# Kernel tuning notes

Measured on AMD Instinct MI355X. Metric: run time of the kernel, lower is better.

The kernel has to match this reference:

```python
import jax, jax.numpy as jnp
import numpy as np

E = 512    # len_embeddings
T = 32     # tokennum
H = 256    # hidden_unit
IT = 5     # ICI iterations
B = 4096   # batch
EPS = 1e-6


def setup_inputs() -> dict:
    key = jax.random.key(0)
    k0, k1, k2, k3, k4 = jax.random.split(key, 5)
    x = jax.random.normal(k0, (B, E), dtype=jnp.float32)
    glorot = np.sqrt(2.0 / (E + H)).astype(np.float32)
    w_in = jax.random.normal(k1, (T, E, H), dtype=jnp.float32) * glorot
    w_val = jax.random.normal(k2, (T, E, H), dtype=jnp.float32) * glorot
    # alphas: per-token, per-iteration inhibition strengths (trained; sample nonzero)
    alphas = jax.random.uniform(k3, (T, IT), dtype=jnp.float32) * 0.5
    # scales: per-token output scale (init 1.0, perturb slightly)
    scales = 1.0 + 0.1 * jax.random.normal(k4, (T, H), dtype=jnp.float32)
    gamma = jnp.ones((T, H), dtype=jnp.float32)
    beta = jnp.zeros((T, H), dtype=jnp.float32)
    return {"x": x, "w_in": w_in, "w_val": w_val, "alphas": alphas,
            "scales": scales, "gamma": gamma, "beta": beta}


def reference(x, w_in, w_val, alphas, scales, gamma, beta):
    # batched per-token projection: [B,E] x [T,E,H] -> [B,T,H]
    hidden = jnp.einsum('be,teh->bth', x, w_in)
    # iterative competitive inhibition (fixed small IT loop)
    x_t = jax.nn.relu(hidden)
    for i in range(alphas.shape[1]):
        m = jnp.mean(x_t, axis=-1, keepdims=True)          # [B,T,1]
        a = alphas[:, i][None, :, None]                     # [1,T,1]
        x_t = jax.nn.relu(x_t - a * m)
    sparse_g = scales[None] * x_t                           # [B,T,H]
    # gated value path
    value = jnp.einsum('be,teh->bth', x, w_val)
    s = sparse_g * value
    # per-token LayerNorm over hidden dim, eps=1e-6
    mu = jnp.mean(s, axis=-1, keepdims=True)
    var = jnp.mean((s - mu) ** 2, axis=-1, keepdims=True)
    out = (s - mu) / jnp.sqrt(var + EPS) * gamma[None] + beta[None]
    return out  # [B, T, H]
```

## Files before the change

### kernel.cpp

```cpp
#include <hip/hip_runtime.h>
#include <cstdint>

using u16 = unsigned short;
using u32 = unsigned int;

constexpr int kB  = 4096;
constexpr int kE  = 512;
constexpr int kT  = 32;
constexpr int kH  = 256;
constexpr int kIT = 5;
constexpr float kEPS = 1e-6f;

typedef __attribute__((ext_vector_type(8)))  short short8;
typedef __attribute__((ext_vector_type(16))) float floatx16;
typedef __attribute__((ext_vector_type(8)))  u16   ushort8;
typedef __attribute__((ext_vector_type(4)))  float floatv4;

__device__ __forceinline__ u16 f2bf(float f) {
  u32 u = __builtin_bit_cast(u32, f);
  return (u16)((u + 0x7fffu + ((u >> 16) & 1u)) >> 16);
}

__device__ __forceinline__ floatx16 mfma32(short8 a, short8 b, floatx16 c) {
  return __builtin_amdgcn_mfma_f32_32x32x16_bf16(a, b, c, 0, 0, 0);
}

__device__ __forceinline__ void ntstore4(float* p, float4 v) {
  __builtin_nontemporal_store(__builtin_bit_cast(floatv4, v), (floatv4*)p);
}

__global__ __launch_bounds__(256) void pack_x_kernel(
    const float* __restrict__ x, u16* __restrict__ xp) {
  __shared__ __attribute__((aligned(16))) float tile[64 * 132];
  const int slab = blockIdx.x >> 2;
  const int kg   = blockIdx.x & 3;
  const int tid  = threadIdx.x;

  const int r0 = tid >> 5;
  const int c0 = (tid & 31) * 4;
#pragma unroll
  for (int p = 0; p < 8; ++p) {
    const int r = p * 8 + r0;
    const float4 v = *(const float4*)(x + (size_t)(slab * 64 + r) * kE + kg * 128 + c0);
    *(float4*)(tile + r * 132 + c0) = v;
  }
  __syncthreads();

  const int wv = tid >> 6, lane = tid & 63;
#pragma unroll
  for (int q = 0; q < 4; ++q) {
    const int cc   = wv * 4 + q;
    const int ks_l = cc >> 1;
    const int mt   = cc & 1;
    const int rl   = mt * 32 + (lane & 31);
    const int kl   = ks_l * 16 + (lane >> 5) * 8;
    const float4 f0 = *(const float4*)(tile + rl * 132 + kl);
    const float4 f1 = *(const float4*)(tile + rl * 132 + kl + 4);
    ushort8 o;
    o[0] = f2bf(f0.x); o[1] = f2bf(f0.y); o[2] = f2bf(f0.z); o[3] = f2bf(f0.w);
    o[4] = f2bf(f1.x); o[5] = f2bf(f1.y); o[6] = f2bf(f1.z); o[7] = f2bf(f1.w);
    const int c = slab * 64 + (kg * 8 + ks_l) * 2 + mt;
    *(ushort8*)(xp + (size_t)c * 512 + lane * 8) = o;
  }
}

__global__ __launch_bounds__(256) void pack_w_kernel(
    const float* __restrict__ w_in, const float* __restrict__ w_val,
    u16* __restrict__ wp) {
  __shared__ __attribute__((aligned(16))) float tile[64 * 68];
  const int wb   = blockIdx.x;
  const int tl   = wb & 31;
  const int et   = tl >> 2;
  const int ht   = tl & 3;
  const int tm   = wb >> 5;
  const int t    = tm >> 1, mat = tm & 1;
  const int tid  = threadIdx.x;
  const float* src = (mat ? w_val : w_in) + (size_t)t * kE * kH +
                     (size_t)(et * 64) * kH + ht * 64;
  const int lrow = tid >> 4, lc4 = (tid & 15) * 4;
#pragma unroll
  for (int p = 0; p < 4; ++p) {
    const int e = lrow + p * 16;
    const float4 v = *(const float4*)(src + (size_t)e * kH + lc4);
    tile[e * 68 + lc4 + 0] = v.x; tile[e * 68 + lc4 + 1] = v.y;
    tile[e * 68 + lc4 + 2] = v.z; tile[e * 68 + lc4 + 3] = v.w;
  }
  __syncthreads();
  const int ks_l = tid >> 6, lane = tid & 63;
  const int kloc = ks_l * 16 + (lane >> 5) * 8;
#pragma unroll
  for (int nt_l = 0; nt_l < 2; ++nt_l) {
    const int nloc = nt_l * 32 + (lane & 31);
    ushort8 o;
#pragma unroll
    for (int j = 0; j < 8; ++j) o[j] = f2bf(tile[(kloc + j) * 68 + nloc]);
    const int c = t * 512 + (et * 4 + ks_l) * 16 + (ht * 2 + nt_l) * 2 + mat;
    *(ushort8*)(wp + (size_t)c * 512 + lane * 8) = o;
  }
}

__global__ __launch_bounds__(512, 4) void fused_kernel(
    const u16* __restrict__ xp, const u16* __restrict__ wp,
    const float* __restrict__ alphas, const float* __restrict__ scales,
    const float* __restrict__ gamma, const float* __restrict__ beta,
    float* __restrict__ out) {
  __shared__ __attribute__((aligned(16))) float sAcc[32 * 256];

  const int tid  = threadIdx.x;
  const int wv   = tid >> 6;
  const int lane = tid & 63;
  const int l31  = lane & 31;
  const int h    = lane >> 5;

  const int bid  = blockIdx.x;
  const int xcd  = bid & 7;
  const int r_   = bid >> 3;
  const int st   = r_ >> 6;
  const int wi   = r_ & 63;
  const int t    = xcd * 4 + (wi >> 4);
  const int slab = st * 16 + (wi & 15);

  const u16* xsrc = xp + (size_t)slab * (32 * 2 * 512) + lane * 8;
  const u16* bsrc = wp + (size_t)t * (32 * 16 * 512) + (size_t)(wv * 2) * 512 + lane * 8;

  floatx16 ai[2], av[2];
#pragma unroll
  for (int m = 0; m < 2; ++m) { ai[m] = (floatx16)0.f; av[m] = (floatx16)0.f; }

  short8 A0[2], A1[2], BI[2], BV[2];
#pragma unroll
  for (int pb = 0; pb < 2; ++pb) {
    A0[pb] = *(const short8*)(xsrc + pb * 1024);
    A1[pb] = *(const short8*)(xsrc + pb * 1024 + 512);
    BI[pb] = *(const short8*)(bsrc + (size_t)pb * 8192);
    BV[pb] = *(const short8*)(bsrc + (size_t)pb * 8192 + 512);
  }

#pragma unroll
  for (int p = 0; p < 32; ++p) {
    const int cur = p & 1;
    ai[0] = mfma32(A0[cur], BI[cur], ai[0]);
    ai[1] = mfma32(A1[cur], BI[cur], ai[1]);
    av[0] = mfma32(A0[cur], BV[cur], av[0]);
    av[1] = mfma32(A1[cur], BV[cur], av[1]);
    if (p < 30) {
      A0[cur] = *(const short8*)(xsrc + (p + 2) * 1024);
      A1[cur] = *(const short8*)(xsrc + (p + 2) * 1024 + 512);
      BI[cur] = *(const short8*)(bsrc + (size_t)(p + 2) * 8192);
      BV[cur] = *(const short8*)(bsrc + (size_t)(p + 2) * 8192 + 512);
    }
  }

  const float inv_h = 1.0f / kH;
  float al[kIT];
#pragma unroll
  for (int i = 0; i < kIT; ++i) al[i] = alphas[t * kIT + i] * inv_h;

  const int row_r = tid >> 4;
  const int seg   = tid & 15;
  const int r4    = (row_r & 7) << 2;

#pragma unroll
  for (int mt = 0; mt < 2; ++mt) {
    __syncthreads();
#pragma unroll
    for (int q = 0; q < 16; ++q) {
      const int r   = (q & 3) + 8 * (q >> 2) + 4 * h;
      const int col = wv * 32 + l31;
      sAcc[r * 256 + (col ^ ((r & 7) << 2))] = ai[mt][q];
    }
    __syncthreads();

    float4 xt[4];
#pragma unroll
    for (int j = 0; j < 4; ++j) {
      xt[j] = *(const float4*)(sAcc + row_r * 256 + ((seg * 16 + 4 * j) ^ r4));
#pragma unroll
      for (int i = 0; i < 4; ++i) xt[j][i] = fmaxf(xt[j][i], 0.f);
    }

#pragma unroll
    for (int it = 0; it < kIT; ++it) {
      float4 s4 = xt[0];
#pragma unroll
      for (int j = 1; j < 4; ++j) s4 += xt[j];
      float v = s4.x + s4.y + s4.z + s4.w;
      v += __shfl_xor(v, 1, 16);
      v += __shfl_xor(v, 2, 16);
      v += __shfl_xor(v, 4, 16);
      v += __shfl_xor(v, 8, 16);
      const float m = al[it] * v;
#pragma unroll
      for (int j = 0; j < 4; ++j)
#pragma unroll
        for (int i = 0; i < 4; ++i) xt[j][i] = fmaxf(xt[j][i] - m, 0.f);
    }

    __syncthreads();
#pragma unroll
    for (int q = 0; q < 16; ++q) {
      const int r   = (q & 3) + 8 * (q >> 2) + 4 * h;
      const int col = wv * 32 + l31;
      sAcc[r * 256 + (col ^ ((r & 7) << 2))] = av[mt][q];
    }
    __syncthreads();

    float4 res[4];
    float sum = 0.f, ssq = 0.f;
#pragma unroll
    for (int j = 0; j < 4; ++j) {
      const int lc = seg * 16 + 4 * j;
      const int cb = lc ^ r4;
      const float4 a4 = *(const float4*)(sAcc + row_r * 256 + cb);
      const float4 sc = *(const float4*)(scales + t * kH + lc);
      float4 s;
#pragma unroll
      for (int i = 0; i < 4; ++i) {
        s[i] = sc[i] * xt[j][i] * a4[i];
        sum += s[i];
        ssq += s[i] * s[i];
      }
      res[j] = s;
    }
    sum += __shfl_xor(sum, 1, 16);  ssq += __shfl_xor(ssq, 1, 16);
    sum += __shfl_xor(sum, 2, 16);  ssq += __shfl_xor(ssq, 2, 16);
    sum += __shfl_xor(sum, 4, 16);  ssq += __shfl_xor(ssq, 4, 16);
    sum += __shfl_xor(sum, 8, 16);  ssq += __shfl_xor(ssq, 8, 16);
    const float mu  = sum * inv_h;
    const float var = ssq * inv_h - mu * mu;
    const float rs  = rsqrtf(var + kEPS);

#pragma unroll
    for (int j = 0; j < 4; ++j) {
      const int lc = seg * 16 + 4 * j;
      const int cb = lc ^ r4;
      const float4 g4 = *(const float4*)(gamma + t * kH + lc);
      const float4 b4 = *(const float4*)(beta + t * kH + lc);
      float4 o;
#pragma unroll
      for (int i = 0; i < 4; ++i) o[i] = (res[j][i] - mu) * rs * g4[i] + b4[i];
      *(float4*)(sAcc + row_r * 256 + cb) = o;
    }
    __syncthreads();

#pragma unroll
    for (int r8 = 0; r8 < 4; ++r8) {
      const int rr = wv * 4 + r8;
      const int rb = (rr & 7) << 2;
      const float4 v = *(const float4*)(sAcc + rr * 256 + ((4 * lane) ^ rb));
      ntstore4(out + (size_t)(slab * 64 + mt * 32 + rr) * (kT * kH) + t * kH + 4 * lane, v);
    }
  }
}

extern "C" void kernel_launch(void* const* d_in, const int* in_sizes, int n_in,
                              void* d_out, int out_size, void* d_ws, size_t ws_size,
                              hipStream_t stream) {
  const float* x      = (const float*)d_in[0];
  const float* w_in   = (const float*)d_in[1];
  const float* w_val  = (const float*)d_in[2];
  const float* alphas = (const float*)d_in[3];
  const float* scales = (const float*)d_in[4];
  const float* gamma  = (const float*)d_in[5];
  const float* beta   = (const float*)d_in[6];
  float* out = (float*)d_out;

  u16* xp = (u16*)d_ws;
  u16* wp = xp + (size_t)64 * 32 * 2 * 512;

  pack_x_kernel<<<256, 256, 0, stream>>>(x, xp);
  pack_w_kernel<<<2048, 256, 0, stream>>>(w_in, w_val, wp);
  fused_kernel<<<kT * (kB / 64), 512, 0, stream>>>(xp, wp, alphas, scales,
                                                   gamma, beta, out);
}
```

Baseline: 290.2 us.

## Stage weight tiles in LDS via global_load_lds and re-split warps 2x4

Instead of each wave loading its own weight fragments straight from global memory into registers, the block cooperatively stages each k-step's weight slice into a double-buffered LDS region using direct global-to-LDS loads. The 8 waves are rearranged into a 2x4 grid, so each wave loads one A fragment and reads four B fragments from LDS. This removes redundant global traffic for A across waves. The cost is two block-wide barriers per k-step and reuse of the staging buffer as the epilogue scratch, with manual vmcnt waits that depend on the exact load count.

```diff
diff --git a/kernel.cpp b/kernel.cpp
--- a/kernel.cpp
+++ b/kernel.cpp
@@ -27,6 +27,12 @@
 
 __device__ __forceinline__ void ntstore4(float* p, float4 v) {
   __builtin_nontemporal_store(__builtin_bit_cast(floatv4, v), (floatv4*)p);
+}
+
+__device__ __forceinline__ void gload16(const u16* gsrc, u16* ldst) {
+  __builtin_amdgcn_global_load_lds(
+      (const __attribute__((address_space(1))) u32*)gsrc,
+      (__attribute__((address_space(3))) u32*)ldst, 16, 0, 0);
 }
 
 __global__ __launch_bounds__(256) void pack_x_kernel(
@@ -104,13 +110,16 @@
     const float* __restrict__ alphas, const float* __restrict__ scales,
     const float* __restrict__ gamma, const float* __restrict__ beta,
     float* __restrict__ out) {
-  __shared__ __attribute__((aligned(16))) float sAcc[32 * 256];
+  __shared__ __attribute__((aligned(16))) u16 sB[2][16 * 512];
+  float* sAcc = (float*)sB;
 
   const int tid  = threadIdx.x;
   const int wv   = tid >> 6;
   const int lane = tid & 63;
   const int l31  = lane & 31;
   const int h    = lane >> 5;
+  const int wm   = wv >> 2;
+  const int wn   = wv & 3;
 
   const int bid  = blockIdx.x;
   const int xcd  = bid & 7;
@@ -121,34 +130,47 @@
   const int slab = st * 16 + (wi & 15);
 
   const u16* xsrc = xp + (size_t)slab * (32 * 2 * 512) + lane * 8;
-  const u16* bsrc = wp + (size_t)t * (32 * 16 * 512) + (size_t)(wv * 2) * 512 + lane * 8;
+  const u16* wsrc = wp + (size_t)t * (32 * 16 * 512) + lane * 8;
 
   floatx16 ai[2], av[2];
 #pragma unroll
-  for (int m = 0; m < 2; ++m) { ai[m] = (floatx16)0.f; av[m] = (floatx16)0.f; }
-
-  short8 A0[2], A1[2], BI[2], BV[2];
-#pragma unroll
-  for (int pb = 0; pb < 2; ++pb) {
-    A0[pb] = *(const short8*)(xsrc + pb * 1024);
-    A1[pb] = *(const short8*)(xsrc + pb * 1024 + 512);
-    BI[pb] = *(const short8*)(bsrc + (size_t)pb * 8192);
-    BV[pb] = *(const short8*)(bsrc + (size_t)pb * 8192 + 512);
-  }
+  for (int n = 0; n < 2; ++n) { ai[n] = (floatx16)0.f; av[n] = (floatx16)0.f; }
+
+  short8 A[2];
+
+  auto stageB = [&](int p, int buf) {
+    const int cb = wv * 2;
+    gload16(wsrc + (size_t)(p * 16 + cb) * 512,     &sB[buf][cb * 512]);
+    gload16(wsrc + (size_t)(p * 16 + cb + 1) * 512, &sB[buf][(cb + 1) * 512]);
+  };
+
+  stageB(0, 0);
+  A[0] = *(const short8*)(xsrc + 0 * 1024 + wm * 512);
 
 #pragma unroll
   for (int p = 0; p < 32; ++p) {
-    const int cur = p & 1;
-    ai[0] = mfma32(A0[cur], BI[cur], ai[0]);
-    ai[1] = mfma32(A1[cur], BI[cur], ai[1]);
-    av[0] = mfma32(A0[cur], BV[cur], av[0]);
-    av[1] = mfma32(A1[cur], BV[cur], av[1]);
-    if (p < 30) {
-      A0[cur] = *(const short8*)(xsrc + (p + 2) * 1024);
-      A1[cur] = *(const short8*)(xsrc + (p + 2) * 1024 + 512);
-      BI[cur] = *(const short8*)(bsrc + (size_t)(p + 2) * 8192);
-      BV[cur] = *(const short8*)(bsrc + (size_t)(p + 2) * 8192 + 512);
-    }
+    if (p < 31) {
+      stageB(p + 1, (p + 1) & 1);
+      A[(p + 1) & 1] = *(const short8*)(xsrc + (size_t)(p + 1) * 1024 + wm * 512);
+    }
+    if (p < 31) { asm volatile("s_waitcnt vmcnt(3)" ::: "memory"); }
+    else        { asm volatile("s_waitcnt vmcnt(0)" ::: "memory"); }
+    __builtin_amdgcn_sched_barrier(0);
+    __builtin_amdgcn_s_barrier();
+    __builtin_amdgcn_sched_barrier(0);
+
+    const u16* sBp = &sB[p & 1][0] + lane * 8;
+    const short8 BI0 = *(const short8*)(sBp + ((wn * 2 + 0) * 2 + 0) * 512);
+    const short8 BV0 = *(const short8*)(sBp + ((wn * 2 + 0) * 2 + 1) * 512);
+    const short8 BI1 = *(const short8*)(sBp + ((wn * 2 + 1) * 2 + 0) * 512);
+    const short8 BV1 = *(const short8*)(sBp + ((wn * 2 + 1) * 2 + 1) * 512);
+    const short8 Ac = A[p & 1];
+    ai[0] = mfma32(Ac, BI0, ai[0]);
+    av[0] = mfma32(Ac, BV0, av[0]);
+    ai[1] = mfma32(Ac, BI1, ai[1]);
+    av[1] = mfma32(Ac, BV1, av[1]);
+    __builtin_amdgcn_sched_barrier(0);
+    __builtin_amdgcn_s_barrier();
   }
 
   const float inv_h = 1.0f / kH;
@@ -163,11 +185,15 @@
 #pragma unroll
   for (int mt = 0; mt < 2; ++mt) {
     __syncthreads();
-#pragma unroll
-    for (int q = 0; q < 16; ++q) {
-      const int r   = (q & 3) + 8 * (q >> 2) + 4 * h;
-      const int col = wv * 32 + l31;
-      sAcc[r * 256 + (col ^ ((r & 7) << 2))] = ai[mt][q];
+    if (wm == mt) {
+#pragma unroll
+      for (int nt = 0; nt < 2; ++nt)
+#pragma unroll
+        for (int q = 0; q < 16; ++q) {
+          const int r   = (q & 3) + 8 * (q >> 2) + 4 * h;
+          const int col = wn * 64 + nt * 32 + l31;
+          sAcc[r * 256 + (col ^ ((r & 7) << 2))] = ai[nt][q];
+        }
     }
     __syncthreads();
 
@@ -197,11 +223,15 @@
     }
 
     __syncthreads();
-#pragma unroll
-    for (int q = 0; q < 16; ++q) {
-      const int r   = (q & 3) + 8 * (q >> 2) + 4 * h;
-      const int col = wv * 32 + l31;
-      sAcc[r * 256 + (col ^ ((r & 7) << 2))] = av[mt][q];
+    if (wm == mt) {
+#pragma unroll
+      for (int nt = 0; nt < 2; ++nt)
+#pragma unroll
+        for (int q = 0; q < 16; ++q) {
+          const int r   = (q & 3) + 8 * (q >> 2) + 4 * h;
+          const int col = wn * 64 + nt * 32 + l31;
+          sAcc[r * 256 + (col ^ ((r & 7) << 2))] = av[nt][q];
+        }
     }
     __syncthreads();
 
```

Result: slower. 343.0 us (+18.2%).
